# Kernel tuning notes

Hardware: AMD Instinct MI355X
Metric: run time of the kernel (lower is better)

The kernel has to match this reference:

```python
import jax, jax.numpy as jnp
import numpy as np

N, C, E, H = 100000, 128, 640000, 128


def setup_inputs() -> dict:
    key = jax.random.key(0)
    ks = jax.random.split(key, 8)
    x = jax.random.normal(ks[0], (N, C), dtype=jnp.float32)
    # edges guaranteed to have no self-loops (module removes them then re-adds clean self-loops)
    rol = jax.random.randint(ks[1], (E,), 0, N, dtype=jnp.int32)
    off = jax.random.randint(ks[2], (E,), 1, N, dtype=jnp.int32)
    col = (rol + off) % N
    edge_index = jnp.stack([rol, col])  # [2, E]
    s = 1.0 / np.sqrt(C)
    return {
        "x": x,
        "edge_index": edge_index,
        "W_emb": jax.random.normal(ks[3], (C, C), dtype=jnp.float32) * s,
        "b_emb": jnp.zeros((C,), dtype=jnp.float32),
        "Wa1": jax.random.normal(ks[4], (C, H), dtype=jnp.float32) * s,
        "ba1": jnp.zeros((H,), dtype=jnp.float32),
        "Wa2": jax.random.normal(ks[5], (H, 1), dtype=jnp.float32) * (1.0 / np.sqrt(H)),
        "ba2": jnp.zeros((1,), dtype=jnp.float32),
        "W_upd": jax.random.normal(ks[6], (C, C), dtype=jnp.float32) * s,
        "b_upd": jnp.zeros((C,), dtype=jnp.float32),
    }


def reference(x, edge_index, W_emb, b_emb, Wa1, ba1, Wa2, ba2, W_upd, b_upd):
    n = x.shape[0]
    loops = jnp.arange(n, dtype=edge_index.dtype)
    rol = jnp.concatenate([edge_index[0], loops])  # [E+N]
    col = jnp.concatenate([edge_index[1], loops])

    embedded_x = x @ W_emb + b_emb                     # [N, C]
    diff = x[rol] - x[col]                             # [E+N, C]
    h = jax.nn.leaky_relu(diff @ Wa1 + ba1, 0.01)      # [E+N, H]
    a = h @ Wa2 + ba2                                  # [E+N, 1]

    # segment softmax over incoming edges of each target node (col)
    amax = jax.ops.segment_max(a, col, num_segments=n)     # [N, 1]
    ea = jnp.exp(a - amax[col])
    denom = jax.ops.segment_sum(ea, col, num_segments=n)   # [N, 1]
    w = ea / (denom[col] + 1e-16)                           # [E+N, 1]

    msg = jax.ops.segment_sum(embedded_x[rol] * w, col, num_segments=n)  # [N, C]
    return msg @ W_upd + b_upd
```

## Files before the change

### kernel.cpp

```cpp
#include <hip/hip_runtime.h>
#include <hip/hip_bf16.h>

#define LRELU(t) ((t) > 0.0f ? (t) : 0.01f * (t))
#define LOG2E 1.4426950408889634f

typedef __attribute__((ext_vector_type(8))) short bf16x8;
typedef __attribute__((ext_vector_type(4))) float f32x4;

__device__ __forceinline__ unsigned short f2bf(float f) {
  unsigned u = __float_as_uint(f);
  u += 0x7fff + ((u >> 16) & 1);
  return (unsigned short)(u >> 16);
}
__device__ __forceinline__ float bflo(unsigned u) { return __uint_as_float(u << 16); }
__device__ __forceinline__ float bfhi(unsigned u) { return __uint_as_float(u & 0xffff0000u); }

__device__ __forceinline__ int pilo(int s) {
  return ((s >> 5) << 6) + ((s & 1) << 5) + ((s >> 1) & 15);
}

__global__ __launch_bounds__(256) void wtrans_kernel(
    const float* __restrict__ W_emb, const float* __restrict__ Wa1,
    const float* __restrict__ W_upd, unsigned short* __restrict__ WtA,
    unsigned short* __restrict__ WtU) {
  int i = blockIdx.x * 256 + threadIdx.x;
  if (i < 32768) {
    int n = i >> 7, k = i & 127;
    float v = (n < 128) ? W_emb[k * 128 + n] : Wa1[k * 128 + (n - 128)];
    WtA[i] = f2bf(v);
  } else if (i < 49152) {
    int j = i - 32768;
    int n = j >> 7, k_st = j & 127;
    int s = k_st >> 1;
    int L = pilo(s) + ((k_st & 1) << 4);
    WtU[j] = f2bf(W_upd[L * 128 + n]);
  }
}

__global__ __launch_bounds__(256) void gemm_embP_kernel(
    const float* __restrict__ A, const unsigned short* __restrict__ Wt,
    const float* __restrict__ b_emb, unsigned* __restrict__ embP, int M) {
  const int lane = threadIdx.x & 63;
  const int w = threadIdx.x >> 6;
  const int row0 = blockIdx.x * 64;
  const int ncol0 = w * 64;
  const int lr = lane & 15;
  const int lg = lane >> 4;
  f32x4 acc[4][4];
#pragma unroll
  for (int mf = 0; mf < 4; ++mf)
#pragma unroll
    for (int nf = 0; nf < 4; ++nf) acc[mf][nf] = (f32x4){0.f, 0.f, 0.f, 0.f};

#pragma unroll
  for (int ks = 0; ks < 4; ++ks) {
    const int k0 = ks * 32 + lg * 8;
    bf16x8 bfr[4];
#pragma unroll
    for (int nf = 0; nf < 4; ++nf)
      bfr[nf] = *reinterpret_cast<const bf16x8*>(Wt + (size_t)(ncol0 + nf * 16 + lr) * 128 + k0);
    bf16x8 afr[4];
#pragma unroll
    for (int mf = 0; mf < 4; ++mf) {
      int row = row0 + mf * 16 + lr;
      if (row >= M) row = M - 1;
      const float* ap = A + (size_t)row * 128 + k0;
      float4 a0 = *reinterpret_cast<const float4*>(ap);
      float4 a1 = *reinterpret_cast<const float4*>(ap + 4);
      bf16x8 t;
      t[0] = (short)f2bf(a0.x); t[1] = (short)f2bf(a0.y);
      t[2] = (short)f2bf(a0.z); t[3] = (short)f2bf(a0.w);
      t[4] = (short)f2bf(a1.x); t[5] = (short)f2bf(a1.y);
      t[6] = (short)f2bf(a1.z); t[7] = (short)f2bf(a1.w);
      afr[mf] = t;
    }
#pragma unroll
    for (int mf = 0; mf < 4; ++mf)
#pragma unroll
      for (int nf = 0; nf < 4; ++nf)
        acc[mf][nf] =
            __builtin_amdgcn_mfma_f32_16x16x32_bf16(afr[mf], bfr[nf], acc[mf][nf], 0, 0, 0);
  }
  float blo[2] = {0.f, 0.f}, bhi[2] = {0.f, 0.f};
  if (ncol0 < 128) {
#pragma unroll
    for (int ph = 0; ph < 2; ++ph) {
      int lo = ncol0 + 32 * ph + lr;
      blo[ph] = b_emb[lo];
      bhi[ph] = b_emb[lo + 16];
    }
  }
#pragma unroll
  for (int mf = 0; mf < 4; ++mf) {
#pragma unroll
    for (int r = 0; r < 4; ++r) {
      int row = row0 + mf * 16 + lg * 4 + r;
      if (row < M) {
        unsigned w0 = (unsigned)f2bf(acc[mf][0][r] + blo[0]) |
                      ((unsigned)f2bf(acc[mf][1][r] + bhi[0]) << 16);
        unsigned w1 = (unsigned)f2bf(acc[mf][2][r] + blo[1]) |
                      ((unsigned)f2bf(acc[mf][3][r] + bhi[1]) << 16);
        *reinterpret_cast<uint2*>(embP + (size_t)row * 128 + w * 32 + lr * 2) =
            make_uint2(w0, w1);
      }
    }
  }
}

__global__ __launch_bounds__(256) void gemm_out_kernel(
    const unsigned short* __restrict__ Ab, const unsigned short* __restrict__ Wt,
    const float* __restrict__ b_upd, float* __restrict__ Cout, int M) {
  const int lane = threadIdx.x & 63;
  const int w = threadIdx.x >> 6;
  const int row0 = blockIdx.x * 128 + (w >> 1) * 64;
  const int ncol0 = (w & 1) * 64;
  const int lr = lane & 15;
  const int lg = lane >> 4;
  f32x4 acc[4][4];
#pragma unroll
  for (int mf = 0; mf < 4; ++mf)
#pragma unroll
    for (int nf = 0; nf < 4; ++nf) acc[mf][nf] = (f32x4){0.f, 0.f, 0.f, 0.f};

#pragma unroll
  for (int ks = 0; ks < 4; ++ks) {
    const int k0 = ks * 32 + lg * 8;
    bf16x8 bfr[4];
#pragma unroll
    for (int nf = 0; nf < 4; ++nf)
      bfr[nf] = *reinterpret_cast<const bf16x8*>(Wt + (size_t)(ncol0 + nf * 16 + lr) * 128 + k0);
    bf16x8 afr[4];
#pragma unroll
    for (int mf = 0; mf < 4; ++mf) {
      int row = row0 + mf * 16 + lr;
      if (row >= M) row = M - 1;
      afr[mf] = *reinterpret_cast<const bf16x8*>(Ab + (size_t)row * 128 + k0);
    }
#pragma unroll
    for (int mf = 0; mf < 4; ++mf)
#pragma unroll
      for (int nf = 0; nf < 4; ++nf)
        acc[mf][nf] =
            __builtin_amdgcn_mfma_f32_16x16x32_bf16(afr[mf], bfr[nf], acc[mf][nf], 0, 0, 0);
  }
#pragma unroll
  for (int nf = 0; nf < 4; ++nf) {
    int col = ncol0 + nf * 16 + lr;
    float bv = b_upd[col];
#pragma unroll
    for (int mf = 0; mf < 4; ++mf) {
      int rowb = row0 + mf * 16 + lg * 4;
#pragma unroll
      for (int r = 0; r < 4; ++r) {
        int row = rowb + r;
        if (row < M) Cout[(size_t)row * 128 + col] = acc[mf][nf][r] + bv;
      }
    }
  }
}

__global__ void zero_kernel(int* __restrict__ p, int n) {
  int i = blockIdx.x * blockDim.x + threadIdx.x;
  if (i < n) p[i] = 0;
}

__global__ void count_kernel(const int* __restrict__ col, int* __restrict__ counts, int E) {
  int e = blockIdx.x * blockDim.x + threadIdx.x;
  if (e < E) atomicAdd(&counts[col[e]], 1);
}

__global__ __launch_bounds__(1024) void scan1_kernel(const int* __restrict__ counts,
                                                     int* __restrict__ offsets,
                                                     int* __restrict__ bsum, int N, int N1) {
  __shared__ int sh[1024];
  int tid = threadIdx.x;
  int i = blockIdx.x * 1024 + tid;
  int v = (i < N) ? counts[i] : 0;
  sh[tid] = v;
  __syncthreads();
  for (int off = 1; off < 1024; off <<= 1) {
    int tv = (tid >= off) ? sh[tid - off] : 0;
    __syncthreads();
    sh[tid] += tv;
    __syncthreads();
  }
  if (i < N1) offsets[i] = sh[tid] - v;
  if (tid == 1023) bsum[blockIdx.x] = sh[1023];
}

__global__ __launch_bounds__(128) void scan2_kernel(int* __restrict__ bsum, int NB) {
  __shared__ int sh[128];
  int tid = threadIdx.x;
  int v = (tid < NB) ? bsum[tid] : 0;
  sh[tid] = v;
  __syncthreads();
  for (int off = 1; off < 128; off <<= 1) {
    int tv = (tid >= off) ? sh[tid - off] : 0;
    __syncthreads();
    sh[tid] += tv;
    __syncthreads();
  }
  if (tid < NB) bsum[tid] = sh[tid] - v;
}

__global__ __launch_bounds__(1024) void scan3_kernel(int* __restrict__ offsets,
                                                     const int* __restrict__ bsum,
                                                     int* __restrict__ cursor, int N, int N1) {
  int i = blockIdx.x * 1024 + threadIdx.x;
  if (i < N1) {
    int o = offsets[i] + bsum[blockIdx.x];
    offsets[i] = o;
    if (i < N) cursor[i] = o;
  }
}

__global__ __launch_bounds__(64) void prep_kernel(const float* __restrict__ ba1,
                                                  const float* __restrict__ Wa2,
                                                  float* __restrict__ a_self,
                                                  float2* __restrict__ ba1p,
                                                  float2* __restrict__ wa2p) {
  int l = threadIdx.x;
  int d = pilo(l);
  ba1p[l] = make_float2(ba1[d], ba1[d + 16]);
  wa2p[l] = make_float2(Wa2[d] * LOG2E, Wa2[d + 16] * LOG2E);
  float t1 = ba1[l], t2 = ba1[l + 64];
  float v = LRELU(t1) * Wa2[l] + LRELU(t2) * Wa2[l + 64];
#pragma unroll
  for (int off = 32; off > 0; off >>= 1) v += __shfl_xor(v, off);
  if (l == 0) *a_self = v * LOG2E;
}

__global__ void scatter_kernel(const int* __restrict__ rol, const int* __restrict__ col,
                               int* __restrict__ cursor, int* __restrict__ csr_rol, int E) {
  int e = blockIdx.x * blockDim.x + threadIdx.x;
  if (e < E) {
    int pos = atomicAdd(&cursor[col[e]], 1);
    csr_rol[pos] = rol[e];
  }
}

__global__ __launch_bounds__(256) void fused_kernel(
    const int* __restrict__ offsets, const int* __restrict__ csr_rol,
    const unsigned* __restrict__ embP, const float2* __restrict__ ba1p,
    const float2* __restrict__ wa2p, const float* __restrict__ a_self_p,
    unsigned* __restrict__ msgb, int N, int nwt) {
  const int lane = threadIdx.x & 63;
  const int q = lane & 15;
  const int wid = blockIdx.x * (blockDim.x >> 6) + (threadIdx.x >> 6);
  const int g = lane >> 4;
  float2 w4[4], b4[4];
#pragma unroll
  for (int k = 0; k < 4; ++k) {
    w4[k] = wa2p[q * 4 + k];
    b4[k] = ba1p[q * 4 + k];
  }
  const float aself = *a_self_p;

  for (int n = wid; n < N; n += nwt) {
    int j0 = offsets[n], j1 = offsets[n + 1];
    const unsigned* rowp = embP + (size_t)n * 128;
    unsigned ue = rowp[lane];
    uint4 pc4 = *reinterpret_cast<const uint4*>(rowp + 64 + q * 4);
    float pm0 = bflo(pc4.x) - b4[0].x, pm1 = bfhi(pc4.x) - b4[0].y;
    float pm2 = bflo(pc4.y) - b4[1].x, pm3 = bfhi(pc4.y) - b4[1].y;
    float pm4 = bflo(pc4.z) - b4[2].x, pm5 = bfhi(pc4.z) - b4[2].y;
    float pm6 = bflo(pc4.w) - b4[3].x, pm7 = bfhi(pc4.w) - b4[3].y;
    float m = aself, s = 1.0f;
    float ax = bflo(ue), ay = bfhi(ue);

    for (int j = j0; j < j1; j += 4) {
      int jj = j + g;
      int jc = (jj < j1) ? jj : (j1 - 1);
      int r = csr_rol[jc];
      int r0 = __shfl(r, 0), r1 = __shfl(r, 16), r2 = __shfl(r, 32), r3 = __shfl(r, 48);
      unsigned pe0 = embP[(size_t)r0 * 128 + lane];
      unsigned pe1 = embP[(size_t)r1 * 128 + lane];
      unsigned pe2 = embP[(size_t)r2 * 128 + lane];
      unsigned pe3 = embP[(size_t)r3 * 128 + lane];
      uint4 pp4 = *reinterpret_cast<const uint4*>(embP + (size_t)r * 128 + 64 + q * 4);
      float t, v;
      t = bflo(pp4.x) - pm0; t = fmaxf(t, 0.01f * t); v = t * w4[0].x;
      t = bfhi(pp4.x) - pm1; t = fmaxf(t, 0.01f * t); v += t * w4[0].y;
      t = bflo(pp4.y) - pm2; t = fmaxf(t, 0.01f * t); v += t * w4[1].x;
      t = bfhi(pp4.y) - pm3; t = fmaxf(t, 0.01f * t); v += t * w4[1].y;
      t = bflo(pp4.z) - pm4; t = fmaxf(t, 0.01f * t); v += t * w4[2].x;
      t = bfhi(pp4.z) - pm5; t = fmaxf(t, 0.01f * t); v += t * w4[2].y;
      t = bflo(pp4.w) - pm6; t = fmaxf(t, 0.01f * t); v += t * w4[3].x;
      t = bfhi(pp4.w) - pm7; t = fmaxf(t, 0.01f * t); v += t * w4[3].y;
      v += __shfl_xor(v, 1);
      v += __shfl_xor(v, 2);
      v += __shfl_xor(v, 4);
      v += __shfl_xor(v, 8);
      float v0 = __shfl(v, 0);
      float s1 = __shfl(v, 16), s2 = __shfl(v, 32), s3 = __shfl(v, 48);
      float v1 = (j + 1 < j1) ? s1 : -1e30f;
      float v2 = (j + 2 < j1) ? s2 : -1e30f;
      float v3 = (j + 3 < j1) ? s3 : -1e30f;
      float nm = fmaxf(fmaxf(m, fmaxf(v0, v1)), fmaxf(v2, v3));
      float cc = __builtin_exp2f(m - nm);
      float e0 = __builtin_exp2f(v0 - nm), e1 = __builtin_exp2f(v1 - nm);
      float e2 = __builtin_exp2f(v2 - nm), e3 = __builtin_exp2f(v3 - nm);
      s = s * cc + ((e0 + e1) + (e2 + e3));
      ax = ax * cc + ((e0 * bflo(pe0) + e1 * bflo(pe1)) + (e2 * bflo(pe2) + e3 * bflo(pe3)));
      ay = ay * cc + ((e0 * bfhi(pe0) + e1 * bfhi(pe1)) + (e2 * bfhi(pe2) + e3 * bfhi(pe3)));
      m = nm;
    }
    float inv = 1.0f / s;
    msgb[(size_t)n * 64 + lane] =
        (unsigned)f2bf(ax * inv) | ((unsigned)f2bf(ay * inv) << 16);
  }
}

extern "C" void kernel_launch(void* const* d_in, const int* in_sizes, int n_in,
                              void* d_out, int out_size, void* d_ws, size_t ws_size,
                              hipStream_t stream) {
  const float* x     = (const float*)d_in[0];
  const int*   ei    = (const int*)d_in[1];
  const float* W_emb = (const float*)d_in[2];
  const float* b_emb = (const float*)d_in[3];
  const float* Wa1   = (const float*)d_in[4];
  const float* ba1   = (const float*)d_in[5];
  const float* Wa2   = (const float*)d_in[6];
  const float* W_upd = (const float*)d_in[8];
  const float* b_upd = (const float*)d_in[9];
  float* out = (float*)d_out;

  const int N = in_sizes[0] / 128;
  const int E = in_sizes[1] / 2;
  const int* rol = ei;
  const int* col = ei + E;

  char* base = (char*)d_ws;
  size_t off = 0;
  auto carve = [&](size_t bytes) {
    void* p = base + off;
    off = (off + bytes + 255) & ~(size_t)255;
    return p;
  };
  unsigned* embP   = (unsigned*)carve((size_t)N * 128 * 4);
  unsigned* msgb   = (unsigned*)carve((size_t)N * 64 * 4);
  unsigned short* WtA = (unsigned short*)carve(256 * 128 * 2);
  unsigned short* WtU = (unsigned short*)carve(128 * 128 * 2);
  float2*   ba1p   = (float2*)carve(64 * 8);
  float2*   wa2p   = (float2*)carve(64 * 8);
  int*      csr_rol= (int*)carve((size_t)E * 4);
  float*    a_self = (float*)carve(16);
  int*      counts = (int*)carve((size_t)N * 4);
  int*      offsets= (int*)carve((size_t)(N + 1) * 4);
  int*      cursor = (int*)carve((size_t)N * 4);
  int*      bsum   = (int*)carve(128 * 4);
  (void)ws_size;

  const int N1 = N + 1;
  const int NB = (N1 + 1023) / 1024;
  const int SBLK = 2048;
  const int NWT = SBLK * 4;

  zero_kernel<<<(N + 255) / 256, 256, 0, stream>>>(counts, N);
  wtrans_kernel<<<192, 256, 0, stream>>>(W_emb, Wa1, W_upd, WtA, WtU);

  gemm_embP_kernel<<<(N + 63) / 64, 256, 0, stream>>>(x, WtA, b_emb, embP, N);

  count_kernel<<<(E + 255) / 256, 256, 0, stream>>>(col, counts, E);
  scan1_kernel<<<NB, 1024, 0, stream>>>(counts, offsets, bsum, N, N1);
  scan2_kernel<<<1, 128, 0, stream>>>(bsum, NB);
  scan3_kernel<<<NB, 1024, 0, stream>>>(offsets, bsum, cursor, N, N1);
  prep_kernel<<<1, 64, 0, stream>>>(ba1, Wa2, a_self, ba1p, wa2p);
  scatter_kernel<<<(E + 255) / 256, 256, 0, stream>>>(rol, col, cursor, csr_rol, E);

  fused_kernel<<<SBLK, 256, 0, stream>>>(offsets, csr_rol, embP, ba1p, wa2p, a_self, msgb, N,
                                         NWT);

  gemm_out_kernel<<<(N + 127) / 128, 256, 0, stream>>>((const unsigned short*)msgb, WtU, b_upd,
                                                       out, N);
}
```

Measured before the change: 350.1 us.

## Switch pipeline to fp16 with packed dot-product logits and lazy-rescale softmax

Replaces bf16 with fp16 everywhere: a separate kernel pre-converts x to fp16, the GEMMs use f16 MFMA with half the rows per block, and packed biases and weights use pkrtz. The fused edge kernel now has each 16-lane group own a separate edge stream. Groups load 16-byte vectors, compute logits with packed half arithmetic and fdot2, and combine their partial softmax states at the end. It also skips the rescale unless the running max grows by more than 8. The intent is to cut ALU and conversion cost and shuffle traffic in the gather loop. In exchange it adds an extra pass over x and takes on fp16 range and precision risk.

```diff
diff --git a/kernel.cpp b/kernel.cpp
--- a/kernel.cpp
+++ b/kernel.cpp
@@ -1,85 +1,99 @@
 #include <hip/hip_runtime.h>
 #include <hip/hip_bf16.h>
+#include <hip/hip_fp16.h>
 
 #define LRELU(t) ((t) > 0.0f ? (t) : 0.01f * (t))
 #define LOG2E 1.4426950408889634f
 
-typedef __attribute__((ext_vector_type(8))) short bf16x8;
+typedef __attribute__((ext_vector_type(8))) _Float16 half8;
+typedef __attribute__((ext_vector_type(2))) _Float16 half2t;
+typedef __attribute__((ext_vector_type(2))) __fp16 fp16x2;
 typedef __attribute__((ext_vector_type(4))) float f32x4;
 
-__device__ __forceinline__ unsigned short f2bf(float f) {
-  unsigned u = __float_as_uint(f);
-  u += 0x7fff + ((u >> 16) & 1);
-  return (unsigned short)(u >> 16);
-}
-__device__ __forceinline__ float bflo(unsigned u) { return __uint_as_float(u << 16); }
-__device__ __forceinline__ float bfhi(unsigned u) { return __uint_as_float(u & 0xffff0000u); }
+union H8U4 { half8 h; uint4 u; half2t p[4]; };
+
+__device__ __forceinline__ unsigned pkrtz(float a, float b) {
+  union { fp16x2 h; unsigned u; } r;
+  r.h = __builtin_amdgcn_cvt_pkrtz(a, b);
+  return r.u;
+}
 
 __device__ __forceinline__ int pilo(int s) {
   return ((s >> 5) << 6) + ((s & 1) << 5) + ((s >> 1) & 15);
 }
 
+#if __has_builtin(__builtin_amdgcn_fdot2)
+#define FDOT2(a, b, c) __builtin_amdgcn_fdot2((a), (b), (c), false)
+#else
+#define FDOT2(a, b, c) ((c) + (float)(a)[0] * (float)(b)[0] + (float)(a)[1] * (float)(b)[1])
+#endif
+
+__global__ __launch_bounds__(256) void xcvt_kernel(const float4* __restrict__ x,
+                                                   uint4* __restrict__ x16, int n8) {
+  int i = blockIdx.x * 256 + threadIdx.x;
+  if (i >= n8) return;
+  float4 a = x[2 * i], b = x[2 * i + 1];
+  uint4 o;
+  o.x = pkrtz(a.x, a.y);
+  o.y = pkrtz(a.z, a.w);
+  o.z = pkrtz(b.x, b.y);
+  o.w = pkrtz(b.z, b.w);
+  x16[i] = o;
+}
+
 __global__ __launch_bounds__(256) void wtrans_kernel(
     const float* __restrict__ W_emb, const float* __restrict__ Wa1,
-    const float* __restrict__ W_upd, unsigned short* __restrict__ WtA,
-    unsigned short* __restrict__ WtU) {
+    const float* __restrict__ W_upd, _Float16* __restrict__ WtA,
+    _Float16* __restrict__ WtU) {
   int i = blockIdx.x * 256 + threadIdx.x;
   if (i < 32768) {
     int n = i >> 7, k = i & 127;
     float v = (n < 128) ? W_emb[k * 128 + n] : Wa1[k * 128 + (n - 128)];
-    WtA[i] = f2bf(v);
+    WtA[i] = (_Float16)v;
   } else if (i < 49152) {
     int j = i - 32768;
     int n = j >> 7, k_st = j & 127;
     int s = k_st >> 1;
     int L = pilo(s) + ((k_st & 1) << 4);
-    WtU[j] = f2bf(W_upd[L * 128 + n]);
+    WtU[j] = (_Float16)W_upd[L * 128 + n];
   }
 }
 
 __global__ __launch_bounds__(256) void gemm_embP_kernel(
-    const float* __restrict__ A, const unsigned short* __restrict__ Wt,
+    const _Float16* __restrict__ A, const _Float16* __restrict__ Wt,
     const float* __restrict__ b_emb, unsigned* __restrict__ embP, int M) {
   const int lane = threadIdx.x & 63;
   const int w = threadIdx.x >> 6;
-  const int row0 = blockIdx.x * 64;
+  const int row0 = blockIdx.x * 32;
   const int ncol0 = w * 64;
   const int lr = lane & 15;
   const int lg = lane >> 4;
-  f32x4 acc[4][4];
-#pragma unroll
-  for (int mf = 0; mf < 4; ++mf)
+  f32x4 acc[2][4];
+#pragma unroll
+  for (int mf = 0; mf < 2; ++mf)
 #pragma unroll
     for (int nf = 0; nf < 4; ++nf) acc[mf][nf] = (f32x4){0.f, 0.f, 0.f, 0.f};
 
 #pragma unroll
   for (int ks = 0; ks < 4; ++ks) {
     const int k0 = ks * 32 + lg * 8;
-    bf16x8 bfr[4];
+    half8 bfr[4];
 #pragma unroll
     for (int nf = 0; nf < 4; ++nf)
-      bfr[nf] = *reinterpret_cast<const bf16x8*>(Wt + (size_t)(ncol0 + nf * 16 + lr) * 128 + k0);
-    bf16x8 afr[4];
-#pragma unroll
-    for (int mf = 0; mf < 4; ++mf) {
+      bfr[nf] = *reinterpret_cast<const half8*>(Wt + (size_t)(ncol0 + nf * 16 + lr) * 128 + k0);
+    half8 afr[2];
+#pragma unroll
+    for (int mf = 0; mf < 2; ++mf) {
       int row = row0 + mf * 16 + lr;
       if (row >= M) row = M - 1;
-      const float* ap = A + (size_t)row * 128 + k0;
-      float4 a0 = *reinterpret_cast<const float4*>(ap);
-      float4 a1 = *reinterpret_cast<const float4*>(ap + 4);
-      bf16x8 t;
-      t[0] = (short)f2bf(a0.x); t[1] = (short)f2bf(a0.y);
-      t[2] = (short)f2bf(a0.z); t[3] = (short)f2bf(a0.w);
-      t[4] = (short)f2bf(a1.x); t[5] = (short)f2bf(a1.y);
-      t[6] = (short)f2bf(a1.z); t[7] = (short)f2bf(a1.w);
-      afr[mf] = t;
-    }
-#pragma unroll
-    for (int mf = 0; mf < 4; ++mf)
+      afr[mf] = *reinterpret_cast<const half8*>(A + (size_t)row * 128 + k0);
+    }
+#pragma unroll
+    for (int mf = 0; mf < 2; ++mf)
 #pragma unroll
       for (int nf = 0; nf < 4; ++nf)
         acc[mf][nf] =
-            __builtin_amdgcn_mfma_f32_16x16x32_bf16(afr[mf], bfr[nf], acc[mf][nf], 0, 0, 0);
+            __builtin_amdgcn_mfma_f32_16x16x32_f16(afr[mf], bfr[nf], acc[mf][nf], 0, 0, 0);
   }
   float blo[2] = {0.f, 0.f}, bhi[2] = {0.f, 0.f};
   if (ncol0 < 128) {
@@ -91,15 +105,13 @@
     }
   }
 #pragma unroll
-  for (int mf = 0; mf < 4; ++mf) {
+  for (int mf = 0; mf < 2; ++mf) {
 #pragma unroll
     for (int r = 0; r < 4; ++r) {
       int row = row0 + mf * 16 + lg * 4 + r;
       if (row < M) {
-        unsigned w0 = (unsigned)f2bf(acc[mf][0][r] + blo[0]) |
-                      ((unsigned)f2bf(acc[mf][1][r] + bhi[0]) << 16);
-        unsigned w1 = (unsigned)f2bf(acc[mf][2][r] + blo[1]) |
-                      ((unsigned)f2bf(acc[mf][3][r] + bhi[1]) << 16);
+        unsigned w0 = pkrtz(acc[mf][0][r] + blo[0], acc[mf][1][r] + bhi[0]);
+        unsigned w1 = pkrtz(acc[mf][2][r] + blo[1], acc[mf][3][r] + bhi[1]);
         *reinterpret_cast<uint2*>(embP + (size_t)row * 128 + w * 32 + lr * 2) =
             make_uint2(w0, w1);
       }
@@ -108,47 +120,47 @@
 }
 
 __global__ __launch_bounds__(256) void gemm_out_kernel(
-    const unsigned short* __restrict__ Ab, const unsigned short* __restrict__ Wt,
+    const _Float16* __restrict__ Ab, const _Float16* __restrict__ Wt,
     const float* __restrict__ b_upd, float* __restrict__ Cout, int M) {
   const int lane = threadIdx.x & 63;
   const int w = threadIdx.x >> 6;
-  const int row0 = blockIdx.x * 128 + (w >> 1) * 64;
+  const int row0 = blockIdx.x * 64 + (w >> 1) * 32;
   const int ncol0 = (w & 1) * 64;
   const int lr = lane & 15;
   const int lg = lane >> 4;
-  f32x4 acc[4][4];
-#pragma unroll
-  for (int mf = 0; mf < 4; ++mf)
+  f32x4 acc[2][4];
+#pragma unroll
+  for (int mf = 0; mf < 2; ++mf)
 #pragma unroll
     for (int nf = 0; nf < 4; ++nf) acc[mf][nf] = (f32x4){0.f, 0.f, 0.f, 0.f};
 
 #pragma unroll
   for (int ks = 0; ks < 4; ++ks) {
     const int k0 = ks * 32 + lg * 8;
-    bf16x8 bfr[4];
+    half8 bfr[4];
 #pragma unroll
     for (int nf = 0; nf < 4; ++nf)
-      bfr[nf] = *reinterpret_cast<const bf16x8*>(Wt + (size_t)(ncol0 + nf * 16 + lr) * 128 + k0);
-    bf16x8 afr[4];
-#pragma unroll
-    for (int mf = 0; mf < 4; ++mf) {
+      bfr[nf] = *reinterpret_cast<const half8*>(Wt + (size_t)(ncol0 + nf * 16 + lr) * 128 + k0);
+    half8 afr[2];
+#pragma unroll
+    for (int mf = 0; mf < 2; ++mf) {
       int row = row0 + mf * 16 + lr;
       if (row >= M) row = M - 1;
-      afr[mf] = *reinterpret_cast<const bf16x8*>(Ab + (size_t)row * 128 + k0);
-    }
-#pragma unroll
-    for (int mf = 0; mf < 4; ++mf)
+      afr[mf] = *reinterpret_cast<const half8*>(Ab + (size_t)row * 128 + k0);
+    }
+#pragma unroll
+    for (int mf = 0; mf < 2; ++mf)
 #pragma unroll
       for (int nf = 0; nf < 4; ++nf)
         acc[mf][nf] =
-            __builtin_amdgcn_mfma_f32_16x16x32_bf16(afr[mf], bfr[nf], acc[mf][nf], 0, 0, 0);
+            __builtin_amdgcn_mfma_f32_16x16x32_f16(afr[mf], bfr[nf], acc[mf][nf], 0, 0, 0);
   }
 #pragma unroll
   for (int nf = 0; nf < 4; ++nf) {
     int col = ncol0 + nf * 16 + lr;
     float bv = b_upd[col];
 #pragma unroll
-    for (int mf = 0; mf < 4; ++mf) {
+    for (int mf = 0; mf < 2; ++mf) {
       int rowb = row0 + mf * 16 + lg * 4;
 #pragma unroll
       for (int r = 0; r < 4; ++r) {
@@ -217,12 +229,12 @@
 __global__ __launch_bounds__(64) void prep_kernel(const float* __restrict__ ba1,
                                                   const float* __restrict__ Wa2,
                                                   float* __restrict__ a_self,
-                                                  float2* __restrict__ ba1p,
-                                                  float2* __restrict__ wa2p) {
+                                                  unsigned* __restrict__ ba1p,
+                                                  unsigned* __restrict__ wa2p) {
   int l = threadIdx.x;
   int d = pilo(l);
-  ba1p[l] = make_float2(ba1[d], ba1[d + 16]);
-  wa2p[l] = make_float2(Wa2[d] * LOG2E, Wa2[d + 16] * LOG2E);
+  ba1p[l] = pkrtz(ba1[d], ba1[d + 16]);
+  wa2p[l] = pkrtz(Wa2[d] * LOG2E, Wa2[d + 16] * LOG2E);
   float t1 = ba1[l], t2 = ba1[l + 64];
   float v = LRELU(t1) * Wa2[l] + LRELU(t2) * Wa2[l + 64];
 #pragma unroll
@@ -239,75 +251,128 @@
   }
 }
 
+__device__ __forceinline__ float logit8(half8 pp, half8 pm, const H8U4& ww) {
+  half8 t = pp - pm;
+  half8 lt = __builtin_elementwise_max(t, t * (_Float16)0.01f);
+  H8U4 L;
+  L.h = lt;
+  float v = FDOT2(L.p[0], ww.p[0], 0.0f);
+  v = FDOT2(L.p[1], ww.p[1], v);
+  v = FDOT2(L.p[2], ww.p[2], v);
+  v = FDOT2(L.p[3], ww.p[3], v);
+  return v;
+}
+
 __global__ __launch_bounds__(256) void fused_kernel(
     const int* __restrict__ offsets, const int* __restrict__ csr_rol,
-    const unsigned* __restrict__ embP, const float2* __restrict__ ba1p,
-    const float2* __restrict__ wa2p, const float* __restrict__ a_self_p,
-    unsigned* __restrict__ msgb, int N, int nwt) {
+    const uint4* __restrict__ embP4, const unsigned* __restrict__ ba1p,
+    const unsigned* __restrict__ wa2p, const float* __restrict__ a_self_p,
+    uint4* __restrict__ msgb4, int N, int nwt) {
   const int lane = threadIdx.x & 63;
   const int q = lane & 15;
+  const int g = lane >> 4;
   const int wid = blockIdx.x * (blockDim.x >> 6) + (threadIdx.x >> 6);
-  const int g = lane >> 4;
-  float2 w4[4], b4[4];
-#pragma unroll
-  for (int k = 0; k < 4; ++k) {
-    w4[k] = wa2p[q * 4 + k];
-    b4[k] = ba1p[q * 4 + k];
-  }
+  H8U4 bb, ww;
+  bb.u = reinterpret_cast<const uint4*>(ba1p)[q];
+  ww.u = reinterpret_cast<const uint4*>(wa2p)[q];
   const float aself = *a_self_p;
 
   for (int n = wid; n < N; n += nwt) {
     int j0 = offsets[n], j1 = offsets[n + 1];
-    const unsigned* rowp = embP + (size_t)n * 128;
-    unsigned ue = rowp[lane];
-    uint4 pc4 = *reinterpret_cast<const uint4*>(rowp + 64 + q * 4);
-    float pm0 = bflo(pc4.x) - b4[0].x, pm1 = bfhi(pc4.x) - b4[0].y;
-    float pm2 = bflo(pc4.y) - b4[1].x, pm3 = bfhi(pc4.y) - b4[1].y;
-    float pm4 = bflo(pc4.z) - b4[2].x, pm5 = bfhi(pc4.z) - b4[2].y;
-    float pm6 = bflo(pc4.w) - b4[3].x, pm7 = bfhi(pc4.w) - b4[3].y;
-    float m = aself, s = 1.0f;
-    float ax = bflo(ue), ay = bfhi(ue);
-
-    for (int j = j0; j < j1; j += 4) {
-      int jj = j + g;
-      int jc = (jj < j1) ? jj : (j1 - 1);
-      int r = csr_rol[jc];
-      int r0 = __shfl(r, 0), r1 = __shfl(r, 16), r2 = __shfl(r, 32), r3 = __shfl(r, 48);
-      unsigned pe0 = embP[(size_t)r0 * 128 + lane];
-      unsigned pe1 = embP[(size_t)r1 * 128 + lane];
-      unsigned pe2 = embP[(size_t)r2 * 128 + lane];
-      unsigned pe3 = embP[(size_t)r3 * 128 + lane];
-      uint4 pp4 = *reinterpret_cast<const uint4*>(embP + (size_t)r * 128 + 64 + q * 4);
-      float t, v;
-      t = bflo(pp4.x) - pm0; t = fmaxf(t, 0.01f * t); v = t * w4[0].x;
-      t = bfhi(pp4.x) - pm1; t = fmaxf(t, 0.01f * t); v += t * w4[0].y;
-      t = bflo(pp4.y) - pm2; t = fmaxf(t, 0.01f * t); v += t * w4[1].x;
-      t = bfhi(pp4.y) - pm3; t = fmaxf(t, 0.01f * t); v += t * w4[1].y;
-      t = bflo(pp4.z) - pm4; t = fmaxf(t, 0.01f * t); v += t * w4[2].x;
-      t = bfhi(pp4.z) - pm5; t = fmaxf(t, 0.01f * t); v += t * w4[2].y;
-      t = bflo(pp4.w) - pm6; t = fmaxf(t, 0.01f * t); v += t * w4[3].x;
-      t = bfhi(pp4.w) - pm7; t = fmaxf(t, 0.01f * t); v += t * w4[3].y;
+    const uint4* rowN = embP4 + (size_t)n * 32;
+    H8U4 ue, up;
+    ue.u = rowN[q];
+    up.u = rowN[16 + q];
+    half8 pm = up.h - bb.h;
+    float acc[8];
+#pragma unroll
+    for (int k = 0; k < 8; ++k) acc[k] = 0.25f * (float)ue.h[k];
+    float m = aself, s = 0.25f;
+
+    int j = j0 + g;
+    for (; j + 4 < j1; j += 8) {
+      int r0 = csr_rol[j], r1 = csr_rol[j + 4];
+      const uint4* R0 = embP4 + (size_t)r0 * 32;
+      const uint4* R1 = embP4 + (size_t)r1 * 32;
+      H8U4 pe0, pp0, pe1, pp1;
+      pe0.u = R0[q];
+      pp0.u = R0[16 + q];
+      pe1.u = R1[q];
+      pp1.u = R1[16 + q];
+      float v0 = logit8(pp0.h, pm, ww);
+      float v1 = logit8(pp1.h, pm, ww);
+      v0 += __shfl_xor(v0, 1);
+      v1 += __shfl_xor(v1, 1);
+      v0 += __shfl_xor(v0, 2);
+      v1 += __shfl_xor(v1, 2);
+      v0 += __shfl_xor(v0, 4);
+      v1 += __shfl_xor(v1, 4);
+      v0 += __shfl_xor(v0, 8);
+      v1 += __shfl_xor(v1, 8);
+      float d0 = v0 - m, d1 = v1 - m;
+      float dm = fmaxf(d0, d1);
+      if (dm <= 8.0f) {
+        float e0 = __builtin_exp2f(d0), e1 = __builtin_exp2f(d1);
+        s += e0 + e1;
+#pragma unroll
+        for (int k = 0; k < 8; ++k) acc[k] += e0 * (float)pe0.h[k] + e1 * (float)pe1.h[k];
+      } else {
+        float c = __builtin_exp2f(-dm);
+        float e0 = __builtin_exp2f(d0 - dm), e1 = __builtin_exp2f(d1 - dm);
+        s = s * c + e0 + e1;
+#pragma unroll
+        for (int k = 0; k < 8; ++k)
+          acc[k] = acc[k] * c + e0 * (float)pe0.h[k] + e1 * (float)pe1.h[k];
+        m += dm;
+      }
+    }
+    if (j < j1) {
+      int r = csr_rol[j];
+      const uint4* R = embP4 + (size_t)r * 32;
+      H8U4 pe, pp;
+      pe.u = R[q];
+      pp.u = R[16 + q];
+      float v = logit8(pp.h, pm, ww);
       v += __shfl_xor(v, 1);
       v += __shfl_xor(v, 2);
       v += __shfl_xor(v, 4);
       v += __shfl_xor(v, 8);
-      float v0 = __shfl(v, 0);
-      float s1 = __shfl(v, 16), s2 = __shfl(v, 32), s3 = __shfl(v, 48);
-      float v1 = (j + 1 < j1) ? s1 : -1e30f;
-      float v2 = (j + 2 < j1) ? s2 : -1e30f;
-      float v3 = (j + 3 < j1) ? s3 : -1e30f;
-      float nm = fmaxf(fmaxf(m, fmaxf(v0, v1)), fmaxf(v2, v3));
-      float cc = __builtin_exp2f(m - nm);
-      float e0 = __builtin_exp2f(v0 - nm), e1 = __builtin_exp2f(v1 - nm);
-      float e2 = __builtin_exp2f(v2 - nm), e3 = __builtin_exp2f(v3 - nm);
-      s = s * cc + ((e0 + e1) + (e2 + e3));
-      ax = ax * cc + ((e0 * bflo(pe0) + e1 * bflo(pe1)) + (e2 * bflo(pe2) + e3 * bflo(pe3)));
-      ay = ay * cc + ((e0 * bfhi(pe0) + e1 * bfhi(pe1)) + (e2 * bfhi(pe2) + e3 * bfhi(pe3)));
-      m = nm;
-    }
-    float inv = 1.0f / s;
-    msgb[(size_t)n * 64 + lane] =
-        (unsigned)f2bf(ax * inv) | ((unsigned)f2bf(ay * inv) << 16);
+      float d = v - m;
+      if (d <= 8.0f) {
+        float e = __builtin_exp2f(d);
+        s += e;
+#pragma unroll
+        for (int k = 0; k < 8; ++k) acc[k] += e * (float)pe.h[k];
+      } else {
+        float c = __builtin_exp2f(-d);
+        s = s * c + 1.0f;
+#pragma unroll
+        for (int k = 0; k < 8; ++k) acc[k] = acc[k] * c + (float)pe.h[k];
+        m = v;
+      }
+    }
+    float mo = fmaxf(m, __shfl_xor(m, 16));
+    mo = fmaxf(mo, __shfl_xor(mo, 32));
+    float c = __builtin_exp2f(m - mo);
+    float st = s * c;
+    st += __shfl_xor(st, 16);
+    st += __shfl_xor(st, 32);
+#pragma unroll
+    for (int k = 0; k < 8; ++k) {
+      float a = acc[k] * c;
+      a += __shfl_xor(a, 16);
+      a += __shfl_xor(a, 32);
+      acc[k] = a;
+    }
+    float inv = 1.0f / st;
+    if (g == 0) {
+      uint4 o;
+      o.x = pkrtz(acc[0] * inv, acc[1] * inv);
+      o.y = pkrtz(acc[2] * inv, acc[3] * inv);
+      o.z = pkrtz(acc[4] * inv, acc[5] * inv);
+      o.w = pkrtz(acc[6] * inv, acc[7] * inv);
+      msgb4[(size_t)n * 16 + q] = o;
+    }
   }
 }
 
@@ -337,18 +402,19 @@
     off = (off + bytes + 255) & ~(size_t)255;
     return p;
   };
-  unsigned* embP   = (unsigned*)carve((size_t)N * 128 * 4);
-  unsigned* msgb   = (unsigned*)carve((size_t)N * 64 * 4);
-  unsigned short* WtA = (unsigned short*)carve(256 * 128 * 2);
-  unsigned short* WtU = (unsigned short*)carve(128 * 128 * 2);
-  float2*   ba1p   = (float2*)carve(64 * 8);
-  float2*   wa2p   = (float2*)carve(64 * 8);
-  int*      csr_rol= (int*)carve((size_t)E * 4);
-  float*    a_self = (float*)carve(16);
-  int*      counts = (int*)carve((size_t)N * 4);
-  int*      offsets= (int*)carve((size_t)(N + 1) * 4);
-  int*      cursor = (int*)carve((size_t)N * 4);
-  int*      bsum   = (int*)carve(128 * 4);
+  unsigned*  embP  = (unsigned*)carve((size_t)N * 128 * 4);
+  _Float16*  x16   = (_Float16*)carve((size_t)N * 128 * 2);
+  unsigned*  msgb  = (unsigned*)carve((size_t)N * 64 * 4);
+  _Float16*  WtA   = (_Float16*)carve(256 * 128 * 2);
+  _Float16*  WtU   = (_Float16*)carve(128 * 128 * 2);
+  unsigned*  ba1p  = (unsigned*)carve(64 * 4);
+  unsigned*  wa2p  = (unsigned*)carve(64 * 4);
+  int*       csr_rol = (int*)carve((size_t)E * 4);
+  float*     a_self  = (float*)carve(16);
+  int*       counts  = (int*)carve((size_t)N * 4);
+  int*       offsets = (int*)carve((size_t)(N + 1) * 4);
+  int*       cursor  = (int*)carve((size_t)N * 4);
+  int*       bsum    = (int*)carve(128 * 4);
   (void)ws_size;
 
   const int N1 = N + 1;
@@ -358,8 +424,9 @@
 
   zero_kernel<<<(N + 255) / 256, 256, 0, stream>>>(counts, N);
   wtrans_kernel<<<192, 256, 0, stream>>>(W_emb, Wa1, W_upd, WtA, WtU);
-
-  gemm_embP_kernel<<<(N + 63) / 64, 256, 0, stream>>>(x, WtA, b_emb, embP, N);
+  xcvt_kernel<<<(N * 16 + 255) / 256, 256, 0, stream>>>((const float4*)x, (uint4*)x16, N * 16);
+
+  gemm_embP_kernel<<<(N + 31) / 32, 256, 0, stream>>>(x16, WtA, b_emb, embP, N);
 
   count_kernel<<<(E + 255) / 256, 256, 0, stream>>>(col, counts, E);
   scan1_kernel<<<NB, 1024, 0, stream>>>(counts, offsets, bsum, N, N1);
@@ -368,9 +435,8 @@
   prep_kernel<<<1, 64, 0, stream>>>(ba1, Wa2, a_self, ba1p, wa2p);
   scatter_kernel<<<(E + 255) / 256, 256, 0, stream>>>(rol, col, cursor, csr_rol, E);
 
-  fused_kernel<<<SBLK, 256, 0, stream>>>(offsets, csr_rol, embP, ba1p, wa2p, a_self, msgb, N,
-                                         NWT);
-
-  gemm_out_kernel<<<(N + 127) / 128, 256, 0, stream>>>((const unsigned short*)msgb, WtU, b_upd,
-                                                       out, N);
-}
+  fused_kernel<<<SBLK, 256, 0, stream>>>(offsets, csr_rol, (const uint4*)embP, ba1p, wa2p,
+                                         a_self, (uint4*)msgb, N, NWT);
+
+  gemm_out_kernel<<<(N + 63) / 64, 256, 0, stream>>>((const _Float16*)msgb, WtU, b_upd, out, N);
+}
```

Measured after the change: 336.4 us. -3.9%, faster.
